# Performance work log

Measured on AMD Instinct MI355X. Metric: run time of the kernel, lower is better.

Reference implementation:

```python
import jax, jax.numpy as jnp
import numpy as np

B, N, D = 64, 256, 1024
E_T, E_C, TOP_K = 4, 4, 2
E = E_T + E_C
HT = 4 * N      # token-mixer hidden
HC = 4 * D      # channel-mixer hidden
HM = 4 * D      # mlp hidden
EPS = 1e-6


def _ln(x):
    mu = jnp.mean(x, axis=-1, keepdims=True)
    var = jnp.mean(jnp.square(x - mu), axis=-1, keepdims=True)
    return (x - mu) * jax.lax.rsqrt(var + EPS)


def _gelu(x):
    return jax.nn.gelu(x, approximate=True)


def _modulate(x, shift, scale):
    return x * (1.0 + scale[:, None, :]) + shift[:, None, :]


def setup_inputs() -> dict:
    key = jax.random.key(0)
    ks = jax.random.split(key, 20)
    def rn(k, shape, fan_in):
        return (jax.random.normal(k, shape, dtype=jnp.float32) / np.sqrt(fan_in)).astype(jnp.float32)
    return {
        "x": jax.random.normal(ks[0], (B, N, D), dtype=jnp.float32),
        "c": jax.random.normal(ks[1], (B, D), dtype=jnp.float32),
        "w_ada": rn(ks[2], (D, 6 * D), D),
        "b_ada": jnp.zeros((6 * D,), jnp.float32),
        "w_router": rn(ks[3], (D, E), D),
        "tm_w1": rn(ks[4], (E_T, N, HT), N),
        "tm_b1": jnp.zeros((E_T, HT), jnp.float32),
        "tm_w2": rn(ks[5], (E_T, HT, N), HT),
        "tm_b2": jnp.zeros((E_T, N), jnp.float32),
        "cm_w1": rn(ks[6], (E_C, D, HC), D),
        "cm_b1": jnp.zeros((E_C, HC), jnp.float32),
        "cm_w2": rn(ks[7], (E_C, HC, D), HC),
        "cm_b2": jnp.zeros((E_C, D), jnp.float32),
        "mlp_w1": rn(ks[8], (D, HM), D),
        "mlp_b1": jnp.zeros((HM,), jnp.float32),
        "mlp_w2": rn(ks[9], (HM, D), HM),
        "mlp_b2": jnp.zeros((D,), jnp.float32),
    }


def _mixer(h, w_router, tm_w1, tm_b1, tm_w2, tm_b2, cm_w1, cm_b1, cm_w2, cm_b2):
    # per-sample routing on mean-pooled tokens
    r_in = jnp.mean(h, axis=1)                         # (B, D)
    logits = r_in @ w_router                            # (B, E)
    probs = jax.nn.softmax(logits, axis=-1)
    tw, ti = jax.lax.top_k(probs, TOP_K)                # (B, K)
    tw = tw / jnp.sum(tw, axis=-1, keepdims=True)
    # combine weights: (B, E), zero for non-selected experts
    combine = jnp.zeros((h.shape[0], E), h.dtype).at[jnp.arange(h.shape[0])[:, None], ti].add(tw)
    out = jnp.zeros_like(h)
    hT = jnp.swapaxes(h, 1, 2)                          # (B, D, N)
    for e in range(E_T):
        hid = _gelu(jnp.einsum('bdn,nh->bdh', hT, tm_w1[e]) + tm_b1[e])
        oe = jnp.einsum('bdh,hn->bdn', hid, tm_w2[e]) + tm_b2[e]
        out = out + combine[:, e, None, None] * jnp.swapaxes(oe, 1, 2)
    for e in range(E_C):
        hid = _gelu(jnp.einsum('bnd,dh->bnh', h, cm_w1[e]) + cm_b1[e])
        oe = jnp.einsum('bnh,hd->bnd', hid, cm_w2[e]) + cm_b2[e]
        out = out + combine[:, E_T + e, None, None] * oe
    # aux load-balancing loss (top-1 assignment fraction x mean probs)
    frac = jnp.mean(jax.nn.one_hot(ti[:, 0], E, dtype=probs.dtype), axis=0)
    aux = E * jnp.sum(jnp.mean(probs, axis=0) * frac)
    return out, aux


def reference(x, c, w_ada, b_ada, w_router, tm_w1, tm_b1, tm_w2, tm_b2,
              cm_w1, cm_b1, cm_w2, cm_b2, mlp_w1, mlp_b1, mlp_w2, mlp_b2):
    mod = jax.nn.silu(c) @ w_ada + b_ada                # (B, 6D)
    s_msa, sc_msa, g_msa, s_mlp, sc_mlp, g_mlp = jnp.split(mod, 6, axis=1)
    h = _modulate(_ln(x), s_msa, sc_msa)
    mix, aux = _mixer(h, w_router, tm_w1, tm_b1, tm_w2, tm_b2, cm_w1, cm_b1, cm_w2, cm_b2)
    x = x + g_msa[:, None, :] * mix
    h2 = _modulate(_ln(x), s_mlp, sc_mlp)
    m = _gelu(h2 @ mlp_w1 + mlp_b1) @ mlp_w2 + mlp_b2
    x = x + g_mlp[:, None, :] * m
    return x, aux
```

## Files before the change

### kernel.cpp

```cpp
#include <hip/hip_runtime.h>
#include <stdint.h>

typedef unsigned short u16;
typedef __attribute__((ext_vector_type(8))) __bf16 bf16x8;
typedef __attribute__((ext_vector_type(4))) float f32x4;

#define DEV static __device__ __forceinline__

DEV u16 f2b(float f) {
  uint32_t u = __builtin_bit_cast(uint32_t, f);
  u += 0x7fffu + ((u >> 16) & 1u);
  return (u16)(u >> 16);
}
DEV float gelu_f(float x) {
  return 0.5f * x * (1.0f + tanhf(0.7978845608028654f * (x + 0.044715f * x * x * x)));
}
DEV void async_cp16(const void* g, void* l) {
  __builtin_amdgcn_global_load_lds(
      (const __attribute__((address_space(1))) unsigned int*)g,
      (__attribute__((address_space(3))) unsigned int*)l, 16, 0, 0);
}

DEV void gemm_tile(const u16* __restrict__ A, int lda,
                   const u16* __restrict__ B, int ldb, int K,
                   u16* As, u16* Bs, f32x4 acc[4][4]) {
  const int tid = threadIdx.x;
  const int w = tid >> 6;
  const int L = tid & 63;
  const int sr = L >> 2;
  const int sk = (L & 3) * 8;
  const int fm = L & 15;
  const int fk = (L >> 4) * 8;
  const u16* ga0 = A + (size_t)(w * 32 + sr) * lda + sk;
  const u16* ga1 = ga0 + 16 * (size_t)lda;
  const u16* gb0 = B + (size_t)(w * 32 + sr) * ldb + sk;
  const u16* gb1 = gb0 + 16 * (size_t)ldb;
  u16* la0 = As + w * 1024 + L * 8;
  u16* la1 = As + w * 1024 + 512 + L * 8;
  u16* lb0 = Bs + w * 1024 + L * 8;
  u16* lb1 = Bs + w * 1024 + 512 + L * 8;
  const u16* fa = As + ((w & 1) * 64 + fm) * 32 + fk;
  const u16* fb = Bs + ((w >> 1) * 64 + fm) * 32 + fk;
  for (int kt = 0; kt < K; kt += 32) {
    __syncthreads();
    async_cp16(ga0 + kt, la0);
    async_cp16(ga1 + kt, la1);
    async_cp16(gb0 + kt, lb0);
    async_cp16(gb1 + kt, lb1);
    __syncthreads();
    bf16x8 av[4], bv[4];
#pragma unroll
    for (int i = 0; i < 4; ++i) {
      av[i] = *(const bf16x8*)(fa + i * 512);
      bv[i] = *(const bf16x8*)(fb + i * 512);
    }
#pragma unroll
    for (int i = 0; i < 4; ++i)
#pragma unroll
      for (int j = 0; j < 4; ++j)
        acc[i][j] = __builtin_amdgcn_mfma_f32_16x16x32_bf16(av[i], bv[j], acc[i][j], 0, 0, 0);
  }
}

DEV void zero_acc(f32x4 acc[4][4]) {
  f32x4 z = {0.f, 0.f, 0.f, 0.f};
#pragma unroll
  for (int i = 0; i < 4; ++i)
#pragma unroll
    for (int j = 0; j < 4; ++j) acc[i][j] = z;
}

__global__ void k_diag(float* out, float v) {
  if (threadIdx.x == 0 && blockIdx.x == 0) out[0] = v;
}

struct TDesc { const float* src; long dstOff; int R, C, tileStart, tilesX; };
struct TArgs { TDesc d[17]; int n; };

__global__ __launch_bounds__(256) void k_transpose(TArgs a, u16* __restrict__ ws) {
  __shared__ float tl[32][33];
  int bid = blockIdx.x;
  int di = 0;
  for (int i = 1; i < a.n; ++i) di = (bid >= a.d[i].tileStart) ? i : di;
  TDesc dd = a.d[di];
  int lt = bid - dd.tileStart;
  int tx = lt % dd.tilesX, ty = lt / dd.tilesX;
  int cc = threadIdx.x & 31, rr = threadIdx.x >> 5;
  const float* sp = dd.src + (size_t)(ty * 32) * dd.C + tx * 32;
#pragma unroll
  for (int i = 0; i < 4; ++i) tl[rr + 8 * i][cc] = sp[(size_t)(rr + 8 * i) * dd.C + cc];
  __syncthreads();
  u16* dp = ws + dd.dstOff + (size_t)(tx * 32) * dd.R + ty * 32;
#pragma unroll
  for (int i = 0; i < 4; ++i) dp[(size_t)(rr + 8 * i) * dd.R + cc] = f2b(tl[cc][rr + 8 * i]);
}

__global__ __launch_bounds__(256) void k_silu(const float* __restrict__ c, u16* __restrict__ cs) {
  int row = blockIdx.x, t = threadIdx.x;
  float4 v = {0.f, 0.f, 0.f, 0.f};
  if (row < 64) v = ((const float4*)(c + (size_t)row * 1024))[t];
  ushort4 o;
  o.x = f2b(v.x / (1.f + expf(-v.x)));
  o.y = f2b(v.y / (1.f + expf(-v.y)));
  o.z = f2b(v.z / (1.f + expf(-v.z)));
  o.w = f2b(v.w / (1.f + expf(-v.w)));
  ((ushort4*)(cs + (size_t)row * 1024))[t] = o;
}

__global__ __launch_bounds__(256) void k_ada(const u16* __restrict__ cs, const u16* __restrict__ wT,
                                             const float* __restrict__ bada, float* __restrict__ modp) {
  __shared__ u16 As[4096] __attribute__((aligned(16)));
  __shared__ u16 Bs[4096] __attribute__((aligned(16)));
  int tn = blockIdx.x;
  f32x4 acc[4][4]; zero_acc(acc);
  gemm_tile(cs, 1024, wT + (size_t)tn * 131072, 1024, 1024, As, Bs, acc);
  const int tid = threadIdx.x, w = tid >> 6, L = tid & 63;
  const int rb = (w & 1) * 64 + ((L >> 4) << 2), cb = (w >> 1) * 64 + (L & 15);
#pragma unroll
  for (int i = 0; i < 4; ++i)
#pragma unroll
    for (int j = 0; j < 4; ++j) {
      int col = tn * 128 + cb + j * 16;
      float bv = bada[col];
#pragma unroll
      for (int r = 0; r < 4; ++r) {
        int row = rb + i * 16 + r;
        modp[(size_t)row * 6144 + col] = acc[i][j][r] + bv;
      }
    }
}

__global__ __launch_bounds__(256) void k_ln(const float* __restrict__ xin, const float* __restrict__ modp,
                                            u16* __restrict__ hout, float* __restrict__ stats,
                                            int shOff, int scOff) {
  int n = blockIdx.x, b = blockIdx.y, t = threadIdx.x;
  const float* xr = xin + ((size_t)b * 256 + n) * 1024;
  float4 v = ((const float4*)xr)[t];
  float s = v.x + v.y + v.z + v.w;
  float s2 = v.x * v.x + v.y * v.y + v.z * v.z + v.w * v.w;
#pragma unroll
  for (int o = 32; o; o >>= 1) { s += __shfl_down(s, o); s2 += __shfl_down(s2, o); }
  __shared__ float red[8];
  int wv = t >> 6, l = t & 63;
  if (l == 0) { red[wv] = s; red[4 + wv] = s2; }
  __syncthreads();
  float S = red[0] + red[1] + red[2] + red[3];
  float S2 = red[4] + red[5] + red[6] + red[7];
  float mu = S * (1.f / 1024.f);
  float var = S2 * (1.f / 1024.f) - mu * mu;
  float rstd = rsqrtf(var + 1e-6f);
  if (stats != nullptr && t == 0) { stats[b * 256 + n] = mu; stats[16384 + b * 256 + n] = rstd; }
  float4 sh = ((const float4*)(modp + b * 6144 + shOff))[t];
  float4 sc = ((const float4*)(modp + b * 6144 + scOff))[t];
  ushort4 o;
  o.x = f2b(((v.x - mu) * rstd) * (1.f + sc.x) + sh.x);
  o.y = f2b(((v.y - mu) * rstd) * (1.f + sc.y) + sh.y);
  o.z = f2b(((v.z - mu) * rstd) * (1.f + sc.z) + sh.z);
  o.w = f2b(((v.w - mu) * rstd) * (1.f + sc.w) + sh.w);
  ((ushort4*)(hout + ((size_t)b * 256 + n) * 1024))[t] = o;
}

__global__ __launch_bounds__(256) void k_htrans(const u16* __restrict__ h, u16* __restrict__ hT) {
  __shared__ u16 tl[32][33];
  int b = blockIdx.z, d0 = blockIdx.x * 32, n0 = blockIdx.y * 32;
  int c = threadIdx.x & 31, r = threadIdx.x >> 5;
  const u16* src = h + (size_t)b * 262144;
#pragma unroll
  for (int i = 0; i < 4; ++i) tl[r + 8 * i][c] = src[(size_t)(n0 + r + 8 * i) * 1024 + d0 + c];
  __syncthreads();
  u16* dst = hT + (size_t)b * 262144;
#pragma unroll
  for (int i = 0; i < 4; ++i) dst[(size_t)(d0 + r + 8 * i) * 256 + n0 + c] = tl[c][r + 8 * i];
}

__global__ __launch_bounds__(256) void k_rin(const float* __restrict__ x, const float* __restrict__ lns,
                                             const float* __restrict__ modp, float* __restrict__ rin) {
  int b = blockIdx.y, d = blockIdx.x * 256 + threadIdx.x;
  const float* xp = x + (size_t)b * 262144 + d;
  const float* mu = lns + b * 256;
  const float* rs = lns + 16384 + b * 256;
  float s = 0.f;
  for (int n = 0; n < 256; ++n) s += (xp[(size_t)n * 1024] - mu[n]) * rs[n];
  float sc = modp[b * 6144 + 1024 + d], sh = modp[b * 6144 + d];
  rin[b * 1024 + d] = (1.f + sc) * (s * (1.f / 256.f)) + sh;
}

__global__ __launch_bounds__(256) void k_router(const float* __restrict__ rin, const float* __restrict__ wr,
                                                float* __restrict__ probs, float* __restrict__ tw,
                                                int* __restrict__ ti, int* __restrict__ top1) {
  __shared__ float red[256][8];
  int b = blockIdx.x, t = threadIdx.x;
  float a[8];
#pragma unroll
  for (int e = 0; e < 8; ++e) a[e] = 0.f;
  for (int d = t; d < 1024; d += 256) {
    float rv = rin[b * 1024 + d];
    const float* wp = wr + d * 8;
#pragma unroll
    for (int e = 0; e < 8; ++e) a[e] += rv * wp[e];
  }
#pragma unroll
  for (int e = 0; e < 8; ++e) red[t][e] = a[e];
  __syncthreads();
  for (int s = 128; s > 0; s >>= 1) {
    if (t < s)
#pragma unroll
      for (int e = 0; e < 8; ++e) red[t][e] += red[t + s][e];
    __syncthreads();
  }
  if (t == 0) {
    float p[8];
    float m = -1e30f;
    for (int e = 0; e < 8; ++e) m = fmaxf(m, red[0][e]);
    float sum = 0.f;
    for (int e = 0; e < 8; ++e) { p[e] = expf(red[0][e] - m); sum += p[e]; }
    float inv = 1.f / sum;
    for (int e = 0; e < 8; ++e) p[e] *= inv;
    int i1 = 0;
    for (int e = 1; e < 8; ++e) if (p[e] > p[i1]) i1 = e;
    int i2 = -1; float bv = -1e30f;
    for (int e = 0; e < 8; ++e) if (e != i1 && p[e] > bv) { bv = p[e]; i2 = e; }
    float ss = p[i1] + p[i2];
    ti[b * 2] = i1; ti[b * 2 + 1] = i2;
    tw[b * 2] = p[i1] / ss; tw[b * 2 + 1] = p[i2] / ss;
    top1[b] = i1;
    for (int e = 0; e < 8; ++e) probs[b * 8 + e] = p[e];
  }
}

__global__ void k_aux(const float* __restrict__ probs, const int* __restrict__ top1,
                      float* __restrict__ auxout) {
  if (threadIdx.x != 0) return;
  float mp[8], fr[8];
  for (int e = 0; e < 8; ++e) { mp[e] = 0.f; fr[e] = 0.f; }
  for (int b = 0; b < 64; ++b) {
    for (int e = 0; e < 8; ++e) mp[e] += probs[b * 8 + e];
    fr[top1[b]] += 1.f;
  }
  float aux = 0.f;
  for (int e = 0; e < 8; ++e) aux += (mp[e] * (1.f / 64.f)) * (fr[e] * (1.f / 64.f));
  auxout[0] = 8.f * aux;
}

__global__ __launch_bounds__(256) void k_gemm1(const u16* __restrict__ h, const u16* __restrict__ hT,
                                               const u16* __restrict__ tmw1T, const u16* __restrict__ cmw1T,
                                               const float* __restrict__ tm_b1, const float* __restrict__ cm_b1,
                                               const int* __restrict__ ti, u16* __restrict__ hid, int slot0) {
  __shared__ u16 As[4096] __attribute__((aligned(16)));
  __shared__ u16 Bs[4096] __attribute__((aligned(16)));
  int tile = blockIdx.x;
  int slot = slot0 + blockIdx.y;
  int b = slot >> 1;
  int e = ti[slot];
  f32x4 acc[4][4]; zero_acc(acc);
  const int tid = threadIdx.x, w = tid >> 6, L = tid & 63;
  const int rb = (w & 1) * 64 + ((L >> 4) << 2), cb = (w >> 1) * 64 + (L & 15);
  u16* outp = hid + (size_t)blockIdx.y * 1048576;
  if (e < 4) {
    int tm = tile >> 3, tn = tile & 7;
    gemm_tile(hT + (size_t)b * 262144 + (size_t)tm * 128 * 256, 256,
              tmw1T + (size_t)e * 262144 + (size_t)tn * 128 * 256, 256, 256, As, Bs, acc);
    const float* bias = tm_b1 + e * 1024 + tn * 128;
#pragma unroll
    for (int i = 0; i < 4; ++i)
#pragma unroll
      for (int j = 0; j < 4; ++j) {
        int col = cb + j * 16;
        float bv = bias[col];
#pragma unroll
        for (int r = 0; r < 4; ++r) {
          int row = tm * 128 + rb + i * 16 + r;
          outp[(size_t)row * 1024 + tn * 128 + col] = f2b(gelu_f(acc[i][j][r] + bv));
        }
      }
  } else {
    int ec = e - 4;
    int tm = tile >> 5, tn = tile & 31;
    gemm_tile(h + (size_t)b * 262144 + (size_t)tm * 128 * 1024, 1024,
              cmw1T + (size_t)ec * 4194304 + (size_t)tn * 128 * 1024, 1024, 1024, As, Bs, acc);
    const float* bias = cm_b1 + ec * 4096 + tn * 128;
#pragma unroll
    for (int i = 0; i < 4; ++i)
#pragma unroll
      for (int j = 0; j < 4; ++j) {
        int col = cb + j * 16;
        float bv = bias[col];
#pragma unroll
        for (int r = 0; r < 4; ++r) {
          int row = tm * 128 + rb + i * 16 + r;
          outp[(size_t)row * 4096 + tn * 128 + col] = f2b(gelu_f(acc[i][j][r] + bv));
        }
      }
  }
}

__global__ __launch_bounds__(256) void k_gemm2(const u16* __restrict__ hid,
                                               const u16* __restrict__ tmw2T, const u16* __restrict__ cmw2T,
                                               const float* __restrict__ tm_b2, const float* __restrict__ cm_b2,
                                               const int* __restrict__ ti, const float* __restrict__ tw,
                                               const float* __restrict__ x, const float* __restrict__ modp,
                                               float* __restrict__ x1, int b0) {
  __shared__ u16 As[4096] __attribute__((aligned(16)));
  __shared__ u16 Bs[4096] __attribute__((aligned(16)));
  int tm = blockIdx.x >> 3, tn = blockIdx.x & 7;
  int b = b0 + blockIdx.y;
  int e0 = ti[b * 2], e1 = ti[b * 2 + 1];
  float w0 = tw[b * 2], w1v = tw[b * 2 + 1];
  f32x4 acc[4][4]; zero_acc(acc);
  const int tid = threadIdx.x, w = tid >> 6, L = tid & 63;
  const int rb = (w & 1) * 64 + ((L >> 4) << 2), cb = (w >> 1) * 64 + (L & 15);
  const u16* hid0 = hid + (size_t)(2 * blockIdx.y) * 1048576;
  const u16* hid1 = hid0 + 1048576;
  if (e0 < 4)
    gemm_tile(tmw2T + (size_t)e0 * 262144 + (size_t)tm * 128 * 1024, 1024,
              hid0 + (size_t)tn * 128 * 1024, 1024, 1024, As, Bs, acc);
  else
    gemm_tile(hid0 + (size_t)tm * 128 * 4096, 4096,
              cmw2T + (size_t)(e0 - 4) * 4194304 + (size_t)tn * 128 * 4096, 4096, 4096, As, Bs, acc);
  float ratio = w0 / w1v;
#pragma unroll
  for (int i = 0; i < 4; ++i)
#pragma unroll
    for (int j = 0; j < 4; ++j)
#pragma unroll
      for (int r = 0; r < 4; ++r) {
        int rowg = tm * 128 + rb + i * 16 + r;
        int colg = tn * 128 + cb + j * 16;
        float bv = (e0 < 4) ? tm_b2[e0 * 256 + rowg] : cm_b2[(e0 - 4) * 1024 + colg];
        acc[i][j][r] = (acc[i][j][r] + bv) * ratio;
      }
  if (e1 < 4)
    gemm_tile(tmw2T + (size_t)e1 * 262144 + (size_t)tm * 128 * 1024, 1024,
              hid1 + (size_t)tn * 128 * 1024, 1024, 1024, As, Bs, acc);
  else
    gemm_tile(hid1 + (size_t)tm * 128 * 4096, 4096,
              cmw2T + (size_t)(e1 - 4) * 4194304 + (size_t)tn * 128 * 4096, 4096, 4096, As, Bs, acc);
  const float* xrow = x + (size_t)b * 262144;
  const float* gm = modp + b * 6144 + 2048;
  float* orow = x1 + (size_t)b * 262144;
#pragma unroll
  for (int i = 0; i < 4; ++i)
#pragma unroll
    for (int j = 0; j < 4; ++j)
#pragma unroll
      for (int r = 0; r < 4; ++r) {
        int rowg = tm * 128 + rb + i * 16 + r;
        int colg = tn * 128 + cb + j * 16;
        float bv = (e1 < 4) ? tm_b2[e1 * 256 + rowg] : cm_b2[(e1 - 4) * 1024 + colg];
        float val = w1v * (acc[i][j][r] + bv);
        size_t idx = (size_t)rowg * 1024 + colg;
        orow[idx] = xrow[idx] + gm[colg] * val;
      }
}

__global__ __launch_bounds__(256) void k_mlp1(const u16* __restrict__ h2, const u16* __restrict__ w1T,
                                              const float* __restrict__ b1, u16* __restrict__ mhid, int r0) {
  __shared__ u16 As[4096] __attribute__((aligned(16)));
  __shared__ u16 Bs[4096] __attribute__((aligned(16)));
  int tn = blockIdx.x, tm = blockIdx.y;
  f32x4 acc[4][4]; zero_acc(acc);
  gemm_tile(h2 + (size_t)(r0 + tm * 128) * 1024, 1024, w1T + (size_t)tn * 131072, 1024, 1024, As, Bs, acc);
  const int tid = threadIdx.x, w = tid >> 6, L = tid & 63;
  const int rb = (w & 1) * 64 + ((L >> 4) << 2), cb = (w >> 1) * 64 + (L & 15);
  const float* bias = b1 + tn * 128;
#pragma unroll
  for (int i = 0; i < 4; ++i)
#pragma unroll
    for (int j = 0; j < 4; ++j) {
      int col = cb + j * 16;
      float bv = bias[col];
#pragma unroll
      for (int r = 0; r < 4; ++r) {
        int row = tm * 128 + rb + i * 16 + r;
        mhid[(size_t)row * 4096 + tn * 128 + col] = f2b(gelu_f(acc[i][j][r] + bv));
      }
    }
}

__global__ __launch_bounds__(256) void k_mlp2(const u16* __restrict__ mhid, const u16* __restrict__ w2T,
                                              const float* __restrict__ b2, const float* __restrict__ modp,
                                              float* __restrict__ xio, int r0) {
  __shared__ u16 As[4096] __attribute__((aligned(16)));
  __shared__ u16 Bs[4096] __attribute__((aligned(16)));
  int tn = blockIdx.x, tm = blockIdx.y;
  f32x4 acc[4][4]; zero_acc(acc);
  gemm_tile(mhid + (size_t)tm * 524288, 4096, w2T + (size_t)tn * 524288, 4096, 4096, As, Bs, acc);
  const int tid = threadIdx.x, w = tid >> 6, L = tid & 63;
  const int rb = (w & 1) * 64 + ((L >> 4) << 2), cb = (w >> 1) * 64 + (L & 15);
#pragma unroll
  for (int i = 0; i < 4; ++i)
#pragma unroll
    for (int j = 0; j < 4; ++j) {
      int col = tn * 128 + cb + j * 16;
      float bv = b2[col];
#pragma unroll
      for (int r = 0; r < 4; ++r) {
        int gr = r0 + tm * 128 + rb + i * 16 + r;
        int bq = gr >> 8;
        size_t idx = (size_t)gr * 1024 + col;
        xio[idx] = xio[idx] + modp[bq * 6144 + 5120 + col] * (acc[i][j][r] + bv);
      }
    }
}

extern "C" void kernel_launch(void* const* d_in, const int* in_sizes, int n_in,
                              void* d_out, int out_size, void* d_ws, size_t ws_size,
                              hipStream_t stream) {
  (void)in_sizes; (void)n_in; (void)out_size;
  const float* x        = (const float*)d_in[0];
  const float* c        = (const float*)d_in[1];
  const float* w_ada    = (const float*)d_in[2];
  const float* b_ada    = (const float*)d_in[3];
  const float* w_router = (const float*)d_in[4];
  const float* tm_w1    = (const float*)d_in[5];
  const float* tm_b1    = (const float*)d_in[6];
  const float* tm_w2    = (const float*)d_in[7];
  const float* tm_b2    = (const float*)d_in[8];
  const float* cm_w1    = (const float*)d_in[9];
  const float* cm_b1    = (const float*)d_in[10];
  const float* cm_w2    = (const float*)d_in[11];
  const float* cm_b2    = (const float*)d_in[12];
  const float* mlp_w1   = (const float*)d_in[13];
  const float* mlp_b1   = (const float*)d_in[14];
  const float* mlp_w2   = (const float*)d_in[15];
  const float* mlp_b2   = (const float*)d_in[16];

  u16* ws16 = (u16*)d_ws;
  char* wsb = (char*)d_ws;
  u16* tmw1T = ws16;
  u16* tmw2T = ws16 + 1048576L;
  u16* cmw1T = ws16 + 2097152L;
  u16* cmw2T = ws16 + 18874368L;
  u16* csilu = ws16 + 35651584L;
  u16* h     = ws16 + 35782656L;
  u16* hT    = ws16 + 52559872L;
  u16* mw1T  = ws16 + 52559872L;
  u16* mw2T  = ws16 + 56754176L;
  float* modp  = (float*)(wsb + 138674176L);
  float* rin   = (float*)(wsb + 141819904L);
  float* probs = (float*)(wsb + 142082048L);
  float* twp   = (float*)(wsb + 142084096L);
  int*   tip   = (int*)(wsb + 142084608L);
  int*   top1p = (int*)(wsb + 142085120L);
  float* lns   = (float*)(wsb + 142085376L);
  const size_t FIXED_END = 142216448ULL;
  u16* tailb = ws16 + FIXED_END / 2;
  float* x1 = (float*)d_out;

  if (ws_size < FIXED_END + 12582912ULL) {
    k_diag<<<1, 64, 0, stream>>>((float*)d_out, (float)(ws_size >> 20));
    return;
  }
  size_t tail = ws_size - FIXED_END;
  int C = 64;
  while ((size_t)C * 4194304ULL > tail) C >>= 1;
  int R = 16384;
  while ((size_t)R * 8192ULL > tail) R >>= 1;

  TArgs t1; int k = 0, start = 0;
#define ADD_T(TA, SRC, DST, RR, CC)                                       \
  do {                                                                    \
    TA.d[k].src = (SRC); TA.d[k].dstOff = (DST);                          \
    TA.d[k].R = (RR); TA.d[k].C = (CC);                                   \
    TA.d[k].tileStart = start; TA.d[k].tilesX = (CC) / 32;                \
    start += ((RR) / 32) * ((CC) / 32); ++k;                              \
  } while (0)
  ADD_T(t1, w_ada, (long)(FIXED_END / 2), 1024, 6144);
  for (int e = 0; e < 4; ++e) ADD_T(t1, tm_w1 + (long)e * 262144, 0L + (long)e * 262144, 256, 1024);
  for (int e = 0; e < 4; ++e) ADD_T(t1, tm_w2 + (long)e * 262144, 1048576L + (long)e * 262144, 1024, 256);
  for (int e = 0; e < 4; ++e) ADD_T(t1, cm_w1 + (long)e * 4194304, 2097152L + (long)e * 4194304, 1024, 4096);
  for (int e = 0; e < 4; ++e) ADD_T(t1, cm_w2 + (long)e * 4194304, 18874368L + (long)e * 4194304, 4096, 1024);
  t1.n = k;
  int t1_tiles = start;

  TArgs t2; k = 0; start = 0;
  ADD_T(t2, mlp_w1, 52559872L, 1024, 4096);
  ADD_T(t2, mlp_w2, 56754176L, 4096, 1024);
  t2.n = k;
  int t2_tiles = start;
#undef ADD_T

  k_transpose<<<dim3(t1_tiles), dim3(256), 0, stream>>>(t1, ws16);
  k_silu<<<dim3(128), dim3(256), 0, stream>>>(c, csilu);
  k_ada<<<dim3(48), dim3(256), 0, stream>>>(csilu, tailb, b_ada, modp);
  k_ln<<<dim3(256, 64), dim3(256), 0, stream>>>(x, modp, h, lns, 0, 1024);
  k_htrans<<<dim3(32, 8, 64), dim3(256), 0, stream>>>(h, hT);
  k_rin<<<dim3(4, 64), dim3(256), 0, stream>>>(x, lns, modp, rin);
  k_router<<<dim3(64), dim3(256), 0, stream>>>(rin, w_router, probs, twp, tip, top1p);
  k_aux<<<dim3(1), dim3(64), 0, stream>>>(probs, top1p, (float*)d_out + 16777216L);
  for (int b0 = 0; b0 < 64; b0 += C) {
    k_gemm1<<<dim3(64, 2 * C), dim3(256), 0, stream>>>(h, hT, tmw1T, cmw1T, tm_b1, cm_b1, tip, tailb, 2 * b0);
    k_gemm2<<<dim3(16, C), dim3(256), 0, stream>>>(tailb, tmw2T, cmw2T, tm_b2, cm_b2, tip, twp, x, modp, x1, b0);
  }
  k_transpose<<<dim3(t2_tiles), dim3(256), 0, stream>>>(t2, ws16);
  k_ln<<<dim3(256, 64), dim3(256), 0, stream>>>(x1, modp, h, nullptr, 3072, 4096);
  for (int r0 = 0; r0 < 16384; r0 += R) {
    k_mlp1<<<dim3(32, R / 128), dim3(256), 0, stream>>>(h, mw1T, mlp_b1, tailb, r0);
    k_mlp2<<<dim3(8, R / 128), dim3(256), 0, stream>>>(tailb, mw2T, mlp_b2, modp, x1, r0);
  }
}
```

Measured before the change: 1.853 ms.

## Triple-buffer LDS in shared GEMM tile with async prefetch two stages ahead

Replaces the single-buffered load-sync-compute loop in gemm_tile with a three-stage ring of LDS buffers. Global-to-LDS async copies are issued two k-steps ahead and gated by explicit vmcnt waits and raw barriers, so memory latency overlaps with MFMA work. LDS use per block triples (48 KB), which can lower occupancy, and the hand-placed waitcnt and barrier ordering risks subtle races.

```diff
diff --git a/kernel.cpp b/kernel.cpp
--- a/kernel.cpp
+++ b/kernel.cpp
@@ -6,6 +6,11 @@
 typedef __attribute__((ext_vector_type(4))) float f32x4;
 
 #define DEV static __device__ __forceinline__
+
+#define VMW8 asm volatile("s_waitcnt vmcnt(8)" ::: "memory")
+#define VMW4 asm volatile("s_waitcnt vmcnt(4)" ::: "memory")
+#define VMW0 asm volatile("s_waitcnt vmcnt(0)" ::: "memory")
+#define LGK0 asm volatile("s_waitcnt lgkmcnt(0)" ::: "memory")
 
 DEV u16 f2b(float f) {
   uint32_t u = __builtin_bit_cast(uint32_t, f);
@@ -35,19 +40,36 @@
   const u16* ga1 = ga0 + 16 * (size_t)lda;
   const u16* gb0 = B + (size_t)(w * 32 + sr) * ldb + sk;
   const u16* gb1 = gb0 + 16 * (size_t)ldb;
-  u16* la0 = As + w * 1024 + L * 8;
-  u16* la1 = As + w * 1024 + 512 + L * 8;
-  u16* lb0 = Bs + w * 1024 + L * 8;
-  u16* lb1 = Bs + w * 1024 + 512 + L * 8;
-  const u16* fa = As + ((w & 1) * 64 + fm) * 32 + fk;
-  const u16* fb = Bs + ((w >> 1) * 64 + fm) * 32 + fk;
-  for (int kt = 0; kt < K; kt += 32) {
-    __syncthreads();
-    async_cp16(ga0 + kt, la0);
-    async_cp16(ga1 + kt, la1);
-    async_cp16(gb0 + kt, lb0);
-    async_cp16(gb1 + kt, lb1);
-    __syncthreads();
+  const int lofs = w * 1024 + L * 8;
+  const int nst = K >> 5;
+
+  VMW0;
+  __syncthreads();
+
+  {
+    u16* la = As + lofs; u16* lb = Bs + lofs;
+    async_cp16(ga0, la); async_cp16(ga1, la + 512);
+    async_cp16(gb0, lb); async_cp16(gb1, lb + 512);
+    la += 4096; lb += 4096;
+    async_cp16(ga0 + 32, la); async_cp16(ga1 + 32, la + 512);
+    async_cp16(gb0 + 32, lb); async_cp16(gb1 + 32, lb + 512);
+  }
+  int s0 = 0, s1 = 4096, s2 = 8192;
+  for (int t = 0; t < nst; ++t) {
+    if (t + 2 < nst) {
+      const int kt = (t + 2) * 32;
+      u16* la = As + s2 + lofs; u16* lb = Bs + s2 + lofs;
+      async_cp16(ga0 + kt, la); async_cp16(ga1 + kt, la + 512);
+      async_cp16(gb0 + kt, lb); async_cp16(gb1 + kt, lb + 512);
+      VMW8;
+    } else if (t + 1 < nst) {
+      VMW4;
+    } else {
+      VMW0;
+    }
+    __builtin_amdgcn_s_barrier();
+    const u16* fa = As + s0 + ((w & 1) * 64 + fm) * 32 + fk;
+    const u16* fb = Bs + s0 + ((w >> 1) * 64 + fm) * 32 + fk;
     bf16x8 av[4], bv[4];
 #pragma unroll
     for (int i = 0; i < 4; ++i) {
@@ -59,6 +81,10 @@
 #pragma unroll
       for (int j = 0; j < 4; ++j)
         acc[i][j] = __builtin_amdgcn_mfma_f32_16x16x32_bf16(av[i], bv[j], acc[i][j], 0, 0, 0);
+    LGK0;
+    __builtin_amdgcn_s_barrier();
+    __builtin_amdgcn_sched_barrier(0);
+    const int tmp = s0; s0 = s1; s1 = s2; s2 = tmp;
   }
 }
 
@@ -109,8 +135,8 @@
 
 __global__ __launch_bounds__(256) void k_ada(const u16* __restrict__ cs, const u16* __restrict__ wT,
                                              const float* __restrict__ bada, float* __restrict__ modp) {
-  __shared__ u16 As[4096] __attribute__((aligned(16)));
-  __shared__ u16 Bs[4096] __attribute__((aligned(16)));
+  __shared__ u16 As[12288] __attribute__((aligned(16)));
+  __shared__ u16 Bs[12288] __attribute__((aligned(16)));
   int tn = blockIdx.x;
   f32x4 acc[4][4]; zero_acc(acc);
   gemm_tile(cs, 1024, wT + (size_t)tn * 131072, 1024, 1024, As, Bs, acc);
@@ -246,8 +272,8 @@
                                                const u16* __restrict__ tmw1T, const u16* __restrict__ cmw1T,
                                                const float* __restrict__ tm_b1, const float* __restrict__ cm_b1,
                                                const int* __restrict__ ti, u16* __restrict__ hid, int slot0) {
-  __shared__ u16 As[4096] __attribute__((aligned(16)));
-  __shared__ u16 Bs[4096] __attribute__((aligned(16)));
+  __shared__ u16 As[12288] __attribute__((aligned(16)));
+  __shared__ u16 Bs[12288] __attribute__((aligned(16)));
   int tile = blockIdx.x;
   int slot = slot0 + blockIdx.y;
   int b = slot >> 1;
@@ -300,8 +326,8 @@
                                                const int* __restrict__ ti, const float* __restrict__ tw,
                                                const float* __restrict__ x, const float* __restrict__ modp,
                                                float* __restrict__ x1, int b0) {
-  __shared__ u16 As[4096] __attribute__((aligned(16)));
-  __shared__ u16 Bs[4096] __attribute__((aligned(16)));
+  __shared__ u16 As[12288] __attribute__((aligned(16)));
+  __shared__ u16 Bs[12288] __attribute__((aligned(16)));
   int tm = blockIdx.x >> 3, tn = blockIdx.x & 7;
   int b = b0 + blockIdx.y;
   int e0 = ti[b * 2], e1 = ti[b * 2 + 1];
@@ -355,8 +381,8 @@
 
 __global__ __launch_bounds__(256) void k_mlp1(const u16* __restrict__ h2, const u16* __restrict__ w1T,
                                               const float* __restrict__ b1, u16* __restrict__ mhid, int r0) {
-  __shared__ u16 As[4096] __attribute__((aligned(16)));
-  __shared__ u16 Bs[4096] __attribute__((aligned(16)));
+  __shared__ u16 As[12288] __attribute__((aligned(16)));
+  __shared__ u16 Bs[12288] __attribute__((aligned(16)));
   int tn = blockIdx.x, tm = blockIdx.y;
   f32x4 acc[4][4]; zero_acc(acc);
   gemm_tile(h2 + (size_t)(r0 + tm * 128) * 1024, 1024, w1T + (size_t)tn * 131072, 1024, 1024, As, Bs, acc);
@@ -380,8 +406,8 @@
 __global__ __launch_bounds__(256) void k_mlp2(const u16* __restrict__ mhid, const u16* __restrict__ w2T,
                                               const float* __restrict__ b2, const float* __restrict__ modp,
                                               float* __restrict__ xio, int r0) {
-  __shared__ u16 As[4096] __attribute__((aligned(16)));
-  __shared__ u16 Bs[4096] __attribute__((aligned(16)));
+  __shared__ u16 As[12288] __attribute__((aligned(16)));
+  __shared__ u16 Bs[12288] __attribute__((aligned(16)));
   int tn = blockIdx.x, tm = blockIdx.y;
   f32x4 acc[4][4]; zero_acc(acc);
   gemm_tile(mhid + (size_t)tm * 524288, 4096, w2T + (size_t)tn * 524288, 4096, 4096, As, Bs, acc);
```

Result: slower. 1.940 ms (+4.7%).
